# Performance work log

Measured on AMD Instinct MI355X. Metric: run time of the kernel, lower is better.

The kernel has to match this reference:

```python
import jax, jax.numpy as jnp
import numpy as np

SCALE = 16
N_CLASSES = 7
IGNORE = -1
MIN_RATIO = 0.75


def setup_inputs() -> dict:
    key = jax.random.key(0)
    # values in [-1, 6]: -1 is the ignore label, 0..6 are classes
    label = jax.random.randint(key, (8, 1024, 1024), 0, N_CLASSES + 1, dtype=jnp.int32) - 1
    return {"label": label}


def reference(label) -> jnp.ndarray:
    bs, H, W = label.shape
    th, tw = H // SCALE, W // SCALE
    # map ignore -> extra class index n_classes
    lab = jnp.where(label == IGNORE, N_CLASSES, label)
    # one-hot [bs, H, W, C+1]; avg_pool2d(kernel=SCALE) == blockwise mean
    oh = jax.nn.one_hot(lab, N_CLASSES + 1, dtype=jnp.float32)
    ratios = oh.reshape(bs, th, SCALE, tw, SCALE, N_CLASSES + 1).mean(axis=(2, 4))  # [bs,th,tw,C+1]
    max_ratio = ratios.max(axis=-1)                      # [bs,th,tw]
    out = ratios.argmax(axis=-1).astype(jnp.int32)       # first-max index, matches torch.max
    out = jnp.where((out == N_CLASSES) | (max_ratio < MIN_RATIO), IGNORE, out)
    return out[:, None, :, :]                            # [bs,1,th,tw]
```

## Files before the change

### kernel.cpp

```cpp
#include <hip/hip_runtime.h>


#define B_ 8
#define H_ 1024
#define W_ 1024
#define TH_ 64
#define TW_ 64

__global__ __launch_bounds__(256) void downscale_label_kernel(
    const int* __restrict__ label, int* __restrict__ out) {
  const int t = threadIdx.x;
  const int bid = blockIdx.x;
  const int b = bid >> 6;
  const int th = bid & 63;

  const size_t base = ((size_t)(b * H_ + th * 16)) * W_ + (size_t)t * 4;
  const int4* p = reinterpret_cast<const int4*>(label + base);

  unsigned long long lo = 0ull, hi = 0ull;
#pragma unroll
  for (int r = 0; r < 16; ++r) {
    const int4 v = p[r * (W_ / 4)];
    const int vals[4] = {v.x, v.y, v.z, v.w};
#pragma unroll
    for (int j = 0; j < 4; ++j) {
      const int cls = vals[j] & 7;
      const unsigned long long inc = 1ull << ((cls & 3) << 4);
      if (cls & 4) hi += inc; else lo += inc;
    }
  }

#pragma unroll
  for (int s = 1; s < 4; s <<= 1) {
    lo += __shfl_xor(lo, s, 64);
    hi += __shfl_xor(hi, s, 64);
  }

  if ((t & 3) == 0) {
    int best = 0;
    int bc = (int)(lo & 0xFFFF);
#pragma unroll
    for (int c = 1; c < 8; ++c) {
      const unsigned long long src = (c < 4) ? lo : hi;
      const int cnt = (int)((src >> ((c & 3) << 4)) & 0xFFFF);
      if (cnt > bc) { bc = cnt; best = c; }
    }
    out[bid * TW_ + (t >> 2)] = (best == 7 || bc < 192) ? -1 : best;
  }
}

extern "C" void kernel_launch(void* const* d_in, const int* in_sizes, int n_in,
                              void* d_out, int out_size, void* d_ws, size_t ws_size,
                              hipStream_t stream) {
  const int* label = (const int*)d_in[0];
  int* out = (int*)d_out;
  downscale_label_kernel<<<B_ * TH_, 256, 0, stream>>>(label, out);
}
```

Before: 70.82 us.

## Split each tile row across four blocks with batched loads and shared-memory reduction

Launches four times as many blocks, each covering a quarter of a 16-row band, and splits the 16 rows across the four wavefronts. Each thread issues its four 16-byte loads up front to keep more memory requests in flight. The per-thread histogram is packed into one 64-bit word with 8-bit counters, which are widened to 16 bits after a cross-wave reduction through shared memory. The cost is a barrier and an LDS round trip per block in return for more memory-level parallelism on a bandwidth-bound read of 32 MB.

```diff
diff --git a/kernel.cpp b/kernel.cpp
--- a/kernel.cpp
+++ b/kernel.cpp
@@ -7,45 +7,58 @@
 #define TH_ 64
 #define TW_ 64
 
-__global__ __launch_bounds__(256) void downscale_label_kernel(
+__global__ __launch_bounds__(256, 8) void downscale_label_kernel(
     const int* __restrict__ label, int* __restrict__ out) {
   const int t = threadIdx.x;
+  const int w = t >> 6;
+  const int l = t & 63;
   const int bid = blockIdx.x;
-  const int b = bid >> 6;
-  const int th = bid & 63;
+  const int q = bid & 3;
+  const int bth = bid >> 2;
 
-  const size_t base = ((size_t)(b * H_ + th * 16)) * W_ + (size_t)t * 4;
-  const int4* p = reinterpret_cast<const int4*>(label + base);
+  const int4* p = reinterpret_cast<const int4*>(
+      label + (size_t)bth * 16 * W_ + (size_t)q * 256 + (size_t)l * 4);
 
-  unsigned long long lo = 0ull, hi = 0ull;
+  int4 v[4];
 #pragma unroll
-  for (int r = 0; r < 16; ++r) {
-    const int4 v = p[r * (W_ / 4)];
-    const int vals[4] = {v.x, v.y, v.z, v.w};
+  for (int r = 0; r < 4; ++r) v[r] = p[(w + r * 4) * (W_ / 4)];
+
+  unsigned long long h = 0ull;
+#pragma unroll
+  for (int r = 0; r < 4; ++r) {
+    const int vals[4] = {v[r].x, v[r].y, v[r].z, v[r].w};
 #pragma unroll
     for (int j = 0; j < 4; ++j) {
       const int cls = vals[j] & 7;
-      const unsigned long long inc = 1ull << ((cls & 3) << 4);
-      if (cls & 4) hi += inc; else lo += inc;
+      h += 1ull << (cls << 3);
     }
   }
 
+  h += __shfl_xor(h, 1, 64);
+  h += __shfl_xor(h, 2, 64);
+
+  __shared__ unsigned long long smem[4][16];
+  if ((l & 3) == 0) smem[w][l >> 2] = h;
+  __syncthreads();
+
+  if (t < 16) {
+    const unsigned long long M = 0x00FF00FF00FF00FFull;
+    unsigned long long e0 = 0ull, e1 = 0ull;
 #pragma unroll
-  for (int s = 1; s < 4; s <<= 1) {
-    lo += __shfl_xor(lo, s, 64);
-    hi += __shfl_xor(hi, s, 64);
-  }
-
-  if ((t & 3) == 0) {
+    for (int ww = 0; ww < 4; ++ww) {
+      const unsigned long long x = smem[ww][t];
+      e0 += x & M;
+      e1 += (x >> 8) & M;
+    }
     int best = 0;
-    int bc = (int)(lo & 0xFFFF);
+    int bc = (int)(e0 & 0xFFFF);
 #pragma unroll
     for (int c = 1; c < 8; ++c) {
-      const unsigned long long src = (c < 4) ? lo : hi;
-      const int cnt = (int)((src >> ((c & 3) << 4)) & 0xFFFF);
+      const unsigned long long src = (c & 1) ? e1 : e0;
+      const int cnt = (int)((src >> ((c >> 1) << 4)) & 0xFFFF);
       if (cnt > bc) { bc = cnt; best = c; }
     }
-    out[bid * TW_ + (t >> 2)] = (best == 7 || bc < 192) ? -1 : best;
+    out[bth * TW_ + q * 16 + t] = (best == 7 || bc < 192) ? -1 : best;
   }
 }
 
@@ -54,5 +67,5 @@
                               hipStream_t stream) {
   const int* label = (const int*)d_in[0];
   int* out = (int*)d_out;
-  downscale_label_kernel<<<B_ * TH_, 256, 0, stream>>>(label, out);
+  downscale_label_kernel<<<B_ * TH_ * 4, 256, 0, stream>>>(label, out);
 }
```

Result: no change. 70.48 us (-0.5%).
